# Optimization experiments

Hardware: AMD Instinct MI355X
Metric: run time of the kernel (lower is better)

Reference implementation:

```python
import jax, jax.numpy as jnp
import numpy as np

NUM_CLASSES = 22
SKIP = 8
INLIER_THR = 0.9
VOTE_THR = 10.0
PERC_THR = 0.02
LABEL_THR = 500
EPS = 1e-8


def setup_inputs() -> dict:
    key = jax.random.key(0)
    k1, k2, k3 = jax.random.split(key, 3)
    N, H, W = 2, 480, 640
    label_2d = jax.random.randint(k1, (N, H, W), 0, NUM_CLASSES).astype(jnp.int32)
    vertex_pred = jax.random.normal(k2, (N, 3 * NUM_CLASSES, H, W), dtype=jnp.float32)
    extents = jax.random.uniform(k3, (NUM_CLASSES, 3), minval=0.05, maxval=0.3, dtype=jnp.float32)
    poses = jnp.zeros((N, 13), dtype=jnp.float32)  # only used when is_train=True
    K = jnp.array([572.4, 0.0, 325.5, 0.0, 573.5, 253.5, 0.0, 0.0, 1.0], dtype=jnp.float32)
    meta_data = jnp.tile(K[None, :], (N, 1))
    return {"label_2d": label_2d, "vertex_pred": vertex_pred, "extents": extents,
            "poses": poses, "meta_data": meta_data}


def _hough(label_2d, vertex_pred, extents, meta_data):
    N, C3, H, W = vertex_pred.shape
    C = NUM_CLASSES
    Hs, Ws = H // SKIP, W // SKIP
    P = Hs * Ws  # subsampled voting pixels == candidate centers

    # subsampled pixel grid coordinates (in full-res pixel units)
    gy, gx = jnp.meshgrid(jnp.arange(Hs) * SKIP, jnp.arange(Ws) * SKIP, indexing='ij')
    px = gx.reshape(-1).astype(jnp.float32)  # [P]
    py = gy.reshape(-1).astype(jnp.float32)  # [P]

    lab = label_2d[:, ::SKIP, ::SKIP].reshape(N, P)                    # [N,P] int
    vp = vertex_pred[:, :, ::SKIP, ::SKIP].reshape(N, C3, P)           # [N,3C,P]

    # label-dependent channel gather: (u,v) center direction + depth z
    idx = (3 * lab)[:, None, :] + jnp.arange(3, dtype=lab.dtype)[None, :, None]  # [N,3,P]
    uvz = jnp.take_along_axis(vp, idx, axis=1)                         # [N,3,P]
    u, v, z = uvz[:, 0], uvz[:, 1], uvz[:, 2]                          # [N,P]

    # pixel -> candidate-center geometry, shared across batch: [P_pix, P_cand]
    dx = px[None, :] - px[:, None]
    dy = py[None, :] - py[:, None]
    dist = jnp.sqrt(dx * dx + dy * dy)

    nrm = jnp.sqrt(u * u + v * v) + EPS                                # [N,P]
    # cosine between predicted direction and actual pixel->candidate direction
    cosang = (u[:, :, None] * dx[None] + v[:, :, None] * dy[None]) / (nrm[:, :, None] * (dist[None] + EPS))

    fg = lab > 0                                                       # background casts no votes
    votes = ((cosang >= INLIER_THR) & (dist[None] > 0) & fg[:, :, None]).astype(jnp.float32)  # [N,P,P]

    # per-class Hough accumulator via scatter over pixel labels
    hough = jax.vmap(lambda vt, l: jax.ops.segment_sum(vt, l, num_segments=C))(votes, lab)  # [N,C,P]
    counts = jax.vmap(lambda l: jax.ops.segment_sum(jnp.ones(l.shape, jnp.float32), l, num_segments=C))(lab)  # [N,C]

    best = jnp.argmax(hough, axis=-1)                                  # [N,C]
    max_votes = jnp.max(hough, axis=-1)                                # [N,C]

    cls_fg = jnp.arange(C)[None, :] > 0
    valid = ((counts * (SKIP * SKIP) >= LABEL_THR)
             & (max_votes >= VOTE_THR)
             & (max_votes >= PERC_THR * counts)
             & cls_fg)

    # inlier clustering: pixels of class c voting for its best center -> mean depth
    v2b = jnp.take_along_axis(votes, best[:, None, :], axis=2)          # [N,P,C]
    onehot = (lab[:, :, None] == jnp.arange(C)[None, None, :]).astype(jnp.float32)
    w = v2b * onehot                                                    # [N,P,C]
    nin = jnp.sum(w, axis=1)                                            # [N,C]
    z_mean = jnp.sum(w * z[:, :, None], axis=1) / jnp.maximum(nin, 1.0)
    zc = jnp.maximum(z_mean, 1e-3)

    cx = jnp.take(px, best)                                             # [N,C]
    cy = jnp.take(py, best)

    fx = meta_data[:, 0:1]; ppx = meta_data[:, 2:3]
    fy = meta_data[:, 4:5]; ppy = meta_data[:, 5:6]

    bw = extents[None, :, 0] * fx / zc                                   # projected box width
    bh = extents[None, :, 1] * fy / zc

    vm = valid.astype(jnp.float32)[..., None]
    bidx = jnp.broadcast_to(jnp.arange(N, dtype=jnp.float32)[:, None], (N, C))
    cidx = jnp.broadcast_to(jnp.arange(C, dtype=jnp.float32)[None, :], (N, C))
    top_box = jnp.stack([bidx, cidx, cx - bw / 2, cy - bh / 2, cx + bw / 2, cy + bh / 2, max_votes], -1) * vm

    tx = (cx - ppx) * zc / fx
    ty = (cy - ppy) * zc / fy
    one = jnp.ones_like(tx); zero = jnp.zeros_like(tx)
    top_pose = jnp.stack([one, zero, zero, zero, tx, ty, zc], -1) * vm   # identity quat + translation
    return top_box, top_pose


def reference(label_2d, vertex_pred, extents, poses, meta_data):
    # poses unused with is_train=False (kept for signature fidelity)
    return _hough(label_2d, vertex_pred, extents, meta_data)
```

## Files before the change

kernel.cpp:

```cpp
#include <hip/hip_runtime.h>

#pragma clang fp contract(off)

#define NCLS 22
#define WS_ 80
#define P 4800
#define NBATCH 2
#define H 480
#define W 640
#define EPSF 1e-8f

#define JTILES 19
#define ICHUNKS 50
#define ILEN 96

__global__ void prep_kernel(const int* __restrict__ label,
                            const float* __restrict__ vp,
                            float4* __restrict__ packed,
                            float2* __restrict__ pos,
                            float* __restrict__ z_s,
                            int4* __restrict__ hough4) {
    int t = blockIdx.x * blockDim.x + threadIdx.x;
    const int nthreads = gridDim.x * blockDim.x;
    const int HTOT4 = NBATCH * NCLS * P / 4;
    for (int q = t; q < HTOT4; q += nthreads) hough4[q] = make_int4(0, 0, 0, 0);

    if (t >= NBATCH * P) return;
    int n = t / P, p = t % P;
    int hs = p / WS_, ws = p % WS_;
    int y = hs * 8, x = ws * 8;
    int lab = label[((size_t)n * H + y) * W + x];
    const size_t HW = (size_t)H * W;
    size_t base = ((size_t)n * (3 * NCLS) + 3 * lab) * HW + (size_t)y * W + x;
    float u = vp[base];
    float v = vp[base + HW];
    float z = vp[base + 2 * HW];
    float nrm = sqrtf(u * u + v * v) + EPSF;
    packed[t] = make_float4(u, v, nrm, __int_as_float(lab));
    pos[t] = make_float2((float)x, (float)y);
    z_s[t] = z;
}

__global__ void __launch_bounds__(256) vote_kernel(
        const float4* __restrict__ packed,
        const float2* __restrict__ pos,
        int* __restrict__ hough) {
    __shared__ float4 sdat[ILEN];
    __shared__ float2 spos[ILEN];
    __shared__ unsigned short hist[NCLS][256];
    int tid = threadIdx.x;
    int j = blockIdx.x * 256 + tid;
    int n = blockIdx.z;
    int i0 = blockIdx.y * ILEN;

    if (tid < ILEN) {
        sdat[tid] = packed[n * P + i0 + tid];
        spos[tid] = pos[n * P + i0 + tid];
    }
    for (int c = 0; c < NCLS; ++c) hist[c][tid] = 0;
    __syncthreads();

    int jc = j < P ? j : 0;
    float pxj = (float)((jc % WS_) * 8);
    float pyj = (float)((jc / WS_) * 8);

    #pragma unroll 4
    for (int ii = 0; ii < ILEN; ++ii) {
        float4 d = sdat[ii];
        int lab = __float_as_int(d.w);
        if (lab == 0) continue;
        float2 pp = spos[ii];
        float dx = pxj - pp.x;
        float dy = pyj - pp.y;
        float d2 = dx * dx + dy * dy;
        float dist = sqrtf(d2);
        float num = d.x * dx + d.y * dy;
        float den = d.z * (dist + EPSF);
        float cosang = num / den;
        int vote = (cosang >= 0.9f) && (d2 > 0.0f);
        hist[lab][tid] += (unsigned short)vote;
    }
    __syncthreads();
    if (j < P) {
        for (int c = 1; c < NCLS; ++c) {
            int h = hist[c][tid];
            if (h) atomicAdd(&hough[((size_t)n * NCLS + c) * P + j], h);
        }
    }
}

__global__ void __launch_bounds__(256) final_kernel(
        const int* __restrict__ hough,
        const float4* __restrict__ packed,
        const float2* __restrict__ pos,
        const float* __restrict__ z_s,
        const float* __restrict__ extents,
        const float* __restrict__ meta,
        float* __restrict__ out) {
    int row_id = blockIdx.x;
    int n = row_id / NCLS, c = row_id % NCLS;
    int tid = threadIdx.x;

    const int* row = &hough[(size_t)row_id * P];
    int bi = tid;
    int bv = row[bi];
    for (int jj = tid + 256; jj < P; jj += 256) {
        int v = row[jj];
        if (v > bv) { bv = v; bi = jj; }
    }
    __shared__ int sv[256], si[256];
    sv[tid] = bv; si[tid] = bi;
    __syncthreads();
    for (int s = 128; s > 0; s >>= 1) {
        if (tid < s) {
            int v2 = sv[tid + s], i2 = si[tid + s];
            if (v2 > sv[tid] || (v2 == sv[tid] && i2 < si[tid])) {
                sv[tid] = v2; si[tid] = i2;
            }
        }
        __syncthreads();
    }
    int b = si[0];
    float mv = (float)sv[0];
    __syncthreads();

    float pxb = (float)((b % WS_) * 8);
    float pyb = (float)((b / WS_) * 8);
    int cnt = 0, nin = 0;
    float zs = 0.0f;
    for (int i = tid; i < P; i += 256) {
        float4 d = packed[n * P + i];
        int lab = __float_as_int(d.w);
        if (lab != c) continue;
        cnt++;
        if (c == 0) continue;
        float2 pp = pos[n * P + i];
        float dx = pxb - pp.x;
        float dy = pyb - pp.y;
        float d2 = dx * dx + dy * dy;
        float dist = sqrtf(d2);
        float num = d.x * dx + d.y * dy;
        float den = d.z * (dist + EPSF);
        float cosang = num / den;
        if ((cosang >= 0.9f) && (d2 > 0.0f)) {
            nin++;
            zs += z_s[n * P + i];
        }
    }
    __shared__ int sc[256], sn[256];
    __shared__ float sz[256];
    sc[tid] = cnt; sn[tid] = nin; sz[tid] = zs;
    __syncthreads();
    for (int s = 128; s > 0; s >>= 1) {
        if (tid < s) {
            sc[tid] += sc[tid + s];
            sn[tid] += sn[tid + s];
            sz[tid] += sz[tid + s];
        }
        __syncthreads();
    }
    if (tid == 0) {
        float cntf = (float)sc[0];
        float ninf = (float)sn[0];
        float z_mean = sz[0] / fmaxf(ninf, 1.0f);
        float zc = fmaxf(z_mean, 0.001f);
        bool valid = (cntf * 64.0f >= 500.0f) && (mv >= 10.0f)
                     && (mv >= 0.02f * cntf) && (c > 0);
        float vm = valid ? 1.0f : 0.0f;
        float fx  = meta[n * 9 + 0];
        float ppx = meta[n * 9 + 2];
        float fy  = meta[n * 9 + 4];
        float ppy = meta[n * 9 + 5];
        float ex = extents[c * 3 + 0];
        float ey = extents[c * 3 + 1];
        float bw = ex * fx / zc;
        float bh = ey * fy / zc;
        float cx = pxb, cy = pyb;
        float tx = (cx - ppx) * zc / fx;
        float ty = (cy - ppy) * zc / fy;
        float* box = out + (size_t)row_id * 7;
        box[0] = (float)n * vm;
        box[1] = (float)c * vm;
        box[2] = (cx - bw / 2.0f) * vm;
        box[3] = (cy - bh / 2.0f) * vm;
        box[4] = (cx + bw / 2.0f) * vm;
        box[5] = (cy + bh / 2.0f) * vm;
        box[6] = mv * vm;
        float* pose = out + (size_t)NBATCH * NCLS * 7 + (size_t)row_id * 7;
        pose[0] = vm;
        pose[1] = 0.0f;
        pose[2] = 0.0f;
        pose[3] = 0.0f;
        pose[4] = tx * vm;
        pose[5] = ty * vm;
        pose[6] = zc * vm;
    }
}

extern "C" void kernel_launch(void* const* d_in, const int* in_sizes, int n_in,
                              void* d_out, int out_size, void* d_ws, size_t ws_size,
                              hipStream_t stream) {
    const int*   label   = (const int*)d_in[0];
    const float* vp      = (const float*)d_in[1];
    const float* extents = (const float*)d_in[2];
    const float* meta    = (const float*)d_in[4];
    float* out = (float*)d_out;

    char* ws = (char*)d_ws;
    float4* packed = (float4*)(ws + 0);
    float2* pos    = (float2*)(ws + 153600);
    float*  z_s    = (float*)(ws + 153600 + 76800);
    int*    hough  = (int*)(ws + 153600 + 76800 + 38400);

    prep_kernel<<<(NBATCH * P + 255) / 256, 256, 0, stream>>>(
        label, vp, packed, pos, z_s, (int4*)hough);

    dim3 vgrid(JTILES, ICHUNKS, NBATCH);
    vote_kernel<<<vgrid, 256, 0, stream>>>(packed, pos, hough);

    final_kernel<<<NBATCH * NCLS, 256, 0, stream>>>(hough, packed, pos, z_s,
                                                    extents, meta, out);
}
```

Baseline: 273.6 us.

## Sort voters by label, use distance lookup table, replace division with multiply compare

Adds a counting-sort kernel that groups the subsampled voting pixels by class label, so each thread can keep one running vote counter and flush it with a single atomic when the label changes, replacing the per-class shared histogram. The sqrt distance is read from a precomputed table indexed by integer grid offsets, which is staged in shared memory. The cosine divide becomes a double-precision multiply-compare against a tuned threshold constant. This removes per-iteration sqrt, divide and histogram read-modify-write, at the cost of an extra serial sort kernel with only two blocks, larger shared memory per block, and double-precision compares whose rounding must match the float reference exactly.

```diff
diff --git a/kernel.cpp b/kernel.cpp
--- a/kernel.cpp
+++ b/kernel.cpp
@@ -4,6 +4,7 @@
 
 #define NCLS 22
 #define WS_ 80
+#define HS_ 60
 #define P 4800
 #define NBATCH 2
 #define H 480
@@ -14,16 +15,29 @@
 #define ICHUNKS 50
 #define ILEN 96
 
+#define TSTRIDE 61
+#define TSIZE (80 * TSTRIDE)
+
+#define MID 0x1.CCCCCBp-1
+
 __global__ void prep_kernel(const int* __restrict__ label,
                             const float* __restrict__ vp,
                             float4* __restrict__ packed,
                             float2* __restrict__ pos,
                             float* __restrict__ z_s,
-                            int4* __restrict__ hough4) {
+                            int4* __restrict__ hough4,
+                            float* __restrict__ tab) {
     int t = blockIdx.x * blockDim.x + threadIdx.x;
     const int nthreads = gridDim.x * blockDim.x;
+
     const int HTOT4 = NBATCH * NCLS * P / 4;
     for (int q = t; q < HTOT4; q += nthreads) hough4[q] = make_int4(0, 0, 0, 0);
+
+    for (int q = t; q < TSIZE; q += nthreads) {
+        int a = q / TSTRIDE, b = q % TSTRIDE;
+        float d2f = (float)(64 * (a * a + b * b));
+        tab[q] = sqrtf(d2f) + EPSF;
+    }
 
     if (t >= NBATCH * P) return;
     int n = t / P, p = t % P;
@@ -41,52 +55,82 @@
     z_s[t] = z;
 }
 
+__global__ void __launch_bounds__(256) sort_kernel(
+        const float4* __restrict__ packed,
+        float4* __restrict__ sorted) {
+    int n = blockIdx.x;
+    int tid = threadIdx.x;
+    __shared__ int cnt[NCLS];
+    __shared__ int cur[NCLS];
+    if (tid < NCLS) cnt[tid] = 0;
+    __syncthreads();
+    for (int p = tid; p < P; p += 256) {
+        int lab = __float_as_int(packed[n * P + p].w);
+        atomicAdd(&cnt[lab], 1);
+    }
+    __syncthreads();
+    if (tid == 0) {
+        int s = 0;
+        for (int c = 0; c < NCLS; ++c) { cur[c] = s; s += cnt[c]; }
+    }
+    __syncthreads();
+    for (int p = tid; p < P; p += 256) {
+        float4 d = packed[n * P + p];
+        int lab = __float_as_int(d.w);
+        int slot = atomicAdd(&cur[lab], 1);
+        int hs = p / WS_, ws = p % WS_;
+        sorted[n * P + slot] =
+            make_float4(d.x, d.y, d.z,
+                        __int_as_float((lab << 16) | (hs << 8) | ws));
+    }
+}
+
 __global__ void __launch_bounds__(256) vote_kernel(
-        const float4* __restrict__ packed,
-        const float2* __restrict__ pos,
+        const float4* __restrict__ sorted,
+        const float* __restrict__ tab,
         int* __restrict__ hough) {
     __shared__ float4 sdat[ILEN];
-    __shared__ float2 spos[ILEN];
-    __shared__ unsigned short hist[NCLS][256];
+    __shared__ float stab[TSIZE];
     int tid = threadIdx.x;
     int j = blockIdx.x * 256 + tid;
     int n = blockIdx.z;
     int i0 = blockIdx.y * ILEN;
 
-    if (tid < ILEN) {
-        sdat[tid] = packed[n * P + i0 + tid];
-        spos[tid] = pos[n * P + i0 + tid];
-    }
-    for (int c = 0; c < NCLS; ++c) hist[c][tid] = 0;
-    __syncthreads();
-
-    int jc = j < P ? j : 0;
-    float pxj = (float)((jc % WS_) * 8);
-    float pyj = (float)((jc / WS_) * 8);
-
-    #pragma unroll 4
+    for (int q = tid; q < TSIZE; q += 256) stab[q] = tab[q];
+    if (tid < ILEN) sdat[tid] = sorted[n * P + i0 + tid];
+    __syncthreads();
+
+    bool jok = j < P;
+    int jc = jok ? j : 0;
+    int jx = jc % WS_;
+    int jy = jc / WS_;
+    int* hrow = &hough[(size_t)n * NCLS * P + jc];
+
+    int acc = 0;
+    int prevlab = -1;
     for (int ii = 0; ii < ILEN; ++ii) {
         float4 d = sdat[ii];
-        int lab = __float_as_int(d.w);
+        int meta = __float_as_int(d.w);
+        int lab = meta >> 16;
+        if (lab != prevlab) {
+            if (prevlab > 0 && acc && jok) atomicAdd(hrow + prevlab * P, acc);
+            acc = 0;
+            prevlab = lab;
+        }
         if (lab == 0) continue;
-        float2 pp = spos[ii];
-        float dx = pxj - pp.x;
-        float dy = pyj - pp.y;
-        float d2 = dx * dx + dy * dy;
-        float dist = sqrtf(d2);
-        float num = d.x * dx + d.y * dy;
-        float den = d.z * (dist + EPSF);
-        float cosang = num / den;
-        int vote = (cosang >= 0.9f) && (d2 > 0.0f);
-        hist[lab][tid] += (unsigned short)vote;
-    }
-    __syncthreads();
-    if (j < P) {
-        for (int c = 1; c < NCLS; ++c) {
-            int h = hist[c][tid];
-            if (h) atomicAdd(&hough[((size_t)n * NCLS + c) * P + j], h);
-        }
-    }
+        int ix = meta & 0xFF;
+        int iy = (meta >> 8) & 0xFF;
+        int ax = jx - ix;
+        int ay = jy - iy;
+        float t = stab[abs(ax) * TSTRIDE + abs(ay)];
+        float den = d.z * t;
+        float dxf = (float)(ax * 8);
+        float dyf = (float)(ay * 8);
+        float num = d.x * dxf + d.y * dyf;
+        int vote = ((double)num >= MID * (double)den) && ((ax | ay) != 0);
+        acc += vote;
+    }
+    if (prevlab > 0 && acc && jok) atomicAdd(hrow + prevlab * P, acc);
 }
 
 __global__ void __launch_bounds__(256) final_kernel(
@@ -211,12 +255,16 @@
     float2* pos    = (float2*)(ws + 153600);
     float*  z_s    = (float*)(ws + 153600 + 76800);
     int*    hough  = (int*)(ws + 153600 + 76800 + 38400);
+    float4* sorted = (float4*)(ws + 153600 + 76800 + 38400 + 844800);
+    float*  tab    = (float*)(ws + 153600 + 76800 + 38400 + 844800 + 153600);
 
     prep_kernel<<<(NBATCH * P + 255) / 256, 256, 0, stream>>>(
-        label, vp, packed, pos, z_s, (int4*)hough);
+        label, vp, packed, pos, z_s, (int4*)hough, tab);
+
+    sort_kernel<<<NBATCH, 256, 0, stream>>>(packed, sorted);
 
     dim3 vgrid(JTILES, ICHUNKS, NBATCH);
-    vote_kernel<<<vgrid, 256, 0, stream>>>(packed, pos, hough);
+    vote_kernel<<<vgrid, 256, 0, stream>>>(sorted, tab, hough);
 
     final_kernel<<<NBATCH * NCLS, 256, 0, stream>>>(hough, packed, pos, z_s,
                                                     extents, meta, out);
```

After: 269.3 us. About the same (-1.6%).
